# Optimization experiments

Hardware: AMD Instinct MI355X
Metric: run time of the kernel (lower is better)

Reference implementation:

```python
import jax, jax.numpy as jnp
import numpy as np

B, D, C, M = 16384, 512, 1000, 8


def setup_inputs() -> dict:
    key = jax.random.key(0)
    k1, k2, k3, k4 = jax.random.split(key, 4)
    x = jax.random.normal(k1, (B, D), dtype=jnp.float32)
    W = jax.random.normal(k2, (M, D, C), dtype=jnp.float32) * 0.02
    b = jax.random.normal(k3, (M, C), dtype=jnp.float32) * 0.02
    coefs = jax.random.uniform(k4, (M,), dtype=jnp.float32, minval=0.5, maxval=1.5)
    return {"x": x, "W": W, "b": b, "coefs": coefs}


def reference(x, W, b, coefs):
    # Per-model logits: [M, B, C]
    logits = jnp.einsum('bd,mdc->mbc', x, W) + b[:, None, :]
    pos = jnp.argmax(logits, axis=-1)  # [M, B] predicted class per model/sample
    rows = jnp.broadcast_to(jnp.arange(x.shape[0])[None, :], pos.shape)  # [M, B]
    # Weighted vote scatter-add: ans[j, pos[m, j]] += coefs[m]
    ans = jnp.zeros((x.shape[0], W.shape[2]), dtype=jnp.float32)
    ans = ans.at[rows, pos].add(jnp.broadcast_to(coefs[:, None], pos.shape))
    return ans / W.shape[0]
```

## Files before the change

### kernel.cpp

```cpp
#include <hip/hip_runtime.h>

#define B_N 16384
#define D_K 512
#define C_N 1000
#define CP 1024
#define M_N 8
#define GAP_EPS 1e-3f

typedef __attribute__((ext_vector_type(8))) _Float16 f16x8;
typedef __attribute__((ext_vector_type(4))) float f32x4;

typedef const __attribute__((address_space(1))) unsigned int* gptr_t;
typedef __attribute__((address_space(3))) unsigned int* lptr_t;

__device__ __forceinline__ void gload16(const void* g, void* l) {
    __builtin_amdgcn_global_load_lds((gptr_t)g, (lptr_t)l, 16, 0, 0);
}

#define BAR()        asm volatile("s_barrier" ::: "memory")
#define WAIT_LGKM0() asm volatile("s_waitcnt lgkmcnt(0)" ::: "memory")
#define WAIT_VM6()   asm volatile("s_waitcnt vmcnt(6)" ::: "memory")
#define WAIT_VM0()   asm volatile("s_waitcnt vmcnt(0)" ::: "memory")

__device__ __forceinline__ unsigned short h16(float f) {
    _Float16 h = (_Float16)f;
    return *(unsigned short*)&h;
}

__device__ __forceinline__ unsigned fkey32(float f) {
    unsigned u = __float_as_uint(f);
    return (u & 0x80000000u) ? ~u : (u | 0x80000000u);
}


__global__ __launch_bounds__(256) void ve_conv(const float* __restrict__ x,
        const float* __restrict__ W, unsigned short* __restrict__ xf,
        unsigned short* __restrict__ wt, unsigned int* __restrict__ cnts,
        float* __restrict__ out) {
    const int tid = threadIdx.x;
    if (blockIdx.x < 8192) {
        int i = blockIdx.x * 256 + tid;
        if (blockIdx.x == 0 && tid < M_N) cnts[tid] = 0u;
        float4 v = reinterpret_cast<const float4*>(x)[i];
        ushort4 h;
        h.x = h16(v.x); h.y = h16(v.y); h.z = h16(v.z); h.w = h16(v.w);
        reinterpret_cast<ushort4*>(xf)[i] = h;
    } else if (blockIdx.x < 9216) {
        __shared__ float t[64][65];
        const int b = blockIdx.x - 8192;
        const int c0 = (b & 15) * 64, k0 = ((b >> 4) & 7) * 64, m = b >> 7;
#pragma unroll
        for (int p = 0; p < 16; ++p) {
            int idx = p * 256 + tid;
            int kk = idx >> 6, cc = idx & 63;
            int c = c0 + cc;
            t[kk][cc] = (c < C_N) ? W[((size_t)m * D_K + k0 + kk) * C_N + c] : 0.f;
        }
        __syncthreads();
#pragma unroll
        for (int p = 0; p < 4; ++p) {
            int idx = p * 256 + tid;
            int cc = idx >> 4, kq = idx & 15;
            ushort4 h;
            h.x = h16(t[kq * 4 + 0][cc]); h.y = h16(t[kq * 4 + 1][cc]);
            h.z = h16(t[kq * 4 + 2][cc]); h.w = h16(t[kq * 4 + 3][cc]);
            size_t o = ((size_t)m * CP + c0 + cc) * D_K + k0 + kq * 4;
            *reinterpret_cast<ushort4*>(wt + o) = h;
        }
    } else {
        const int b = blockIdx.x - 9216;
        float4* po = reinterpret_cast<float4*>(out) + (size_t)b * 4000;
        const float4 z = make_float4(0.f, 0.f, 0.f, 0.f);
        for (int i = tid; i < 4000; i += 256) po[i] = z;
    }
}


__global__ __launch_bounds__(256, 2) void ve_gemm16d(
        const unsigned short* __restrict__ Xf, const unsigned short* __restrict__ WT,
        const float* __restrict__ bias, float4* __restrict__ part) {
    __shared__ unsigned short At[12288];
    __shared__ unsigned short Bt[24576];

    const int tid = threadIdx.x;
    const int l = tid & 63, w = tid >> 6;
    const int wr = w >> 1, wc = w & 1;
    const int l15 = l & 15, kg = l >> 4;
    const int bid = blockIdx.x;
    const int mb = bid & 7, ct = (bid >> 3) & 3, rt = bid >> 5;
    const int r0 = rt * 128, c0 = ct * 256;

    const int lhi = l >> 3, llo = l & 7;
    const int s3g = llo ^ lhi;
    const int srow16 = (lhi << 1) | (s3g >> 2);
    const int kgs = (s3g & 3) * 8;

    const unsigned short* xA0 = Xf + (size_t)(r0 +      w * 16 + srow16) * D_K + kgs;
    const unsigned short* xA1 = Xf + (size_t)(r0 + 64 + w * 16 + srow16) * D_K + kgs;
    const unsigned short* xB0 = WT + (size_t)(mb * CP + c0 +       w * 16 + srow16) * D_K + kgs;
    const unsigned short* xB1 = WT + (size_t)(mb * CP + c0 +  64 + w * 16 + srow16) * D_K + kgs;
    const unsigned short* xB2 = WT + (size_t)(mb * CP + c0 + 128 + w * 16 + srow16) * D_K + kgs;
    const unsigned short* xB3 = WT + (size_t)(mb * CP + c0 + 192 + w * 16 + srow16) * D_K + kgs;

    auto stage = [&](int t, int buf) {
        unsigned short* A = At + buf * 4096;
        unsigned short* B = Bt + buf * 8192;
        gload16(xA0 + t * 32, A + tid * 8);
        gload16(xA1 + t * 32, A + 2048 + tid * 8);
        gload16(xB0 + t * 32, B + tid * 8);
        gload16(xB1 + t * 32, B + 2048 + tid * 8);
        gload16(xB2 + t * 32, B + 4096 + tid * 8);
        gload16(xB3 + t * 32, B + 6144 + tid * 8);
    };

    auto ldsoff = [&](int row, int kc) {
        return (row >> 1) * 64 + (((((row & 1) << 2) | kc) ^ ((row >> 1) & 7)) * 8);
    };
    const char* aP[4]; const char* bP[8];
#pragma unroll
    for (int i = 0; i < 4; ++i)
        aP[i] = (const char*)At + 2 * ldsoff(wr * 64 + i * 16 + l15, kg);
#pragma unroll
    for (int j = 0; j < 8; ++j)
        bP[j] = (const char*)Bt + wc * 8192 + 2 * ldsoff(j * 16 + l15, kg);

    f32x4 acc[4][8];
#pragma unroll
    for (int i = 0; i < 4; ++i)
#pragma unroll
        for (int j = 0; j < 8; ++j) acc[i][j] = (f32x4){0.f, 0.f, 0.f, 0.f};

    stage(0, 0);
    stage(1, 1);
    WAIT_VM6();
    BAR();

#pragma unroll 1
    for (int t = 0; t < 16; ++t) {
        if (t < 14) stage(t + 2, (t + 2) % 3);
        const int curA = (t % 3) * 8192;
        const int curB = (t % 3) * 16384;

        f16x8 af[4], bf[8];
#pragma unroll
        for (int i = 0; i < 4; ++i) af[i] = *reinterpret_cast<const f16x8*>(aP[i] + curA);
#pragma unroll
        for (int j = 0; j < 8; ++j) bf[j] = *reinterpret_cast<const f16x8*>(bP[j] + curB);
        __builtin_amdgcn_s_setprio(1);
#pragma unroll
        for (int i = 0; i < 4; ++i)
#pragma unroll
            for (int j = 0; j < 8; ++j)
                acc[i][j] = __builtin_amdgcn_mfma_f32_16x16x32_f16(af[i], bf[j], acc[i][j], 0, 0, 0);
        __builtin_amdgcn_s_setprio(0);

        if (t < 14)       { WAIT_VM6(); }
        else if (t == 14) { WAIT_VM0(); }
        WAIT_LGKM0();
        BAR();
    }

    float4 (*wtop)[2] = reinterpret_cast<float4(*)[2]>(At);

    float bv[8]; int cg[8];
#pragma unroll
    for (int j = 0; j < 8; ++j) {
        int c = c0 + wc * 128 + j * 16 + l15;
        cg[j] = c;
        bv[j] = (c < C_N) ? bias[mb * C_N + c] : -1e30f;
    }
#pragma unroll
    for (int i = 0; i < 4; ++i) {
#pragma unroll
        for (int reg = 0; reg < 4; ++reg) {
            float v1 = acc[i][0][reg] + bv[0]; int i1 = cg[0];
            float v2 = -1e30f;
#pragma unroll
            for (int j = 1; j < 8; ++j) {
                float v = acc[i][j][reg] + bv[j];
                float mn = fminf(v, v1);
                v2 = fmaxf(v2, mn);
                i1 = (v > v1) ? cg[j] : i1;
                v1 = fmaxf(v1, v);
            }
#pragma unroll
            for (int mask = 1; mask < 16; mask <<= 1) {
                float ov1 = __shfl_xor(v1, mask);
                int   oi1 = __shfl_xor(i1, mask);
                float ov2 = __shfl_xor(v2, mask);
                float mn = fminf(v1, ov1);
                v2 = fmaxf(fmaxf(v2, ov2), mn);
                i1 = (ov1 > v1) ? oi1 : i1;
                v1 = fmaxf(v1, ov1);
            }
            if (l15 == 0) {
                int row = wr * 64 + i * 16 + (l >> 4) * 4 + reg;
                wtop[row][wc] = make_float4(v1, __int_as_float(i1), v2, 0.f);
            }
        }
    }
    __syncthreads();
    if (tid < 128) {
        float4 a = wtop[tid][0], b = wtop[tid][1];
        float v1, v2; int i1;
        if (b.x > a.x) {
            v1 = b.x; i1 = __float_as_int(b.y);
            v2 = fmaxf(a.x, b.z);
        } else {
            v1 = a.x; i1 = __float_as_int(a.y);
            v2 = fmaxf(b.x, a.z);
        }
        part[((size_t)mb * B_N + r0 + tid) * 4 + ct] =
            make_float4(v1, __int_as_float(i1), v2, 0.f);
    }
}


__global__ __launch_bounds__(128) void ve_flag4(const float4* __restrict__ part,
        unsigned int* __restrict__ wout, unsigned int* __restrict__ rlist,
        unsigned int* __restrict__ cnts, unsigned long long* __restrict__ fixkey) {
    int r = blockIdx.x * 128 + threadIdx.x;
#pragma unroll
    for (int m = 0; m < M_N; ++m) {
        float4 o = part[((size_t)m * B_N + r) * 4 + 0];
        float v1 = o.x; int i1 = __float_as_int(o.y); float v2 = o.z;
#pragma unroll
        for (int t = 1; t < 4; ++t) {
            float4 q = part[((size_t)m * B_N + r) * 4 + t];
            if (q.x > v1) {
                v2 = fmaxf(v1, fmaxf(q.z, v2));
                v1 = q.x; i1 = __float_as_int(q.y);
            } else {
                v2 = fmaxf(v2, q.x);
            }
        }
        if (v1 - v2 <= GAP_EPS) {
            wout[m * B_N + r] = (unsigned)i1 | 0x80000000u;
            fixkey[m * B_N + r] = 0ull;
            unsigned pos = atomicAdd(&cnts[m], 1u);
            rlist[m * B_N + pos] = (unsigned)r;
        } else {
            wout[m * B_N + r] = (unsigned)i1;
        }
    }
}


__global__ __launch_bounds__(256) void ve_exact_g(
        const float* __restrict__ x, const float* __restrict__ W,
        const float* __restrict__ bias, const unsigned int* __restrict__ rlist,
        const unsigned int* __restrict__ cnts, unsigned long long* __restrict__ fixkey) {
    __shared__ float xs[32][65];
    __shared__ float wsm[32][128];
    __shared__ int rg[64];
    const int ct = blockIdx.x, m = blockIdx.z;
    const int tid = threadIdx.x;
    const int tx = tid & 15, ty = tid >> 4;
    const int c0 = ct * 128;
    const unsigned nm = cnts[m];

    for (unsigned rb = blockIdx.y; rb * 64 < nm; rb += gridDim.y) {
        __syncthreads();
        if (tid < 64) {
            unsigned idx = rb * 64 + tid;
            rg[tid] = (idx < nm) ? (int)rlist[m * B_N + idx] : 0;
        }
        __syncthreads();

        float acc[4][8];
#pragma unroll
        for (int i = 0; i < 4; i++)
#pragma unroll
            for (int j = 0; j < 8; j++) acc[i][j] = 0.f;

        for (int kt = 0; kt < D_K; kt += 32) {
#pragma unroll
            for (int i = 0; i < 2; i++) {
                int li = tid + i * 256;
                int row = li >> 3, kq = li & 7;
                float4 v = *reinterpret_cast<const float4*>(
                        x + (size_t)rg[row] * D_K + kt + kq * 4);
                int kk = kq * 4;
                xs[kk + 0][row] = v.x; xs[kk + 1][row] = v.y;
                xs[kk + 2][row] = v.z; xs[kk + 3][row] = v.w;
            }
#pragma unroll
            for (int i = 0; i < 4; i++) {
                int li = tid + i * 256;
                int kk = li >> 5, cq = li & 31;
                int c = c0 + cq * 4;
                const float* p = W + ((size_t)(m * D_K + kt + kk)) * C_N + c;
                float4 v;
                if (c + 3 < C_N) v = *reinterpret_cast<const float4*>(p);
                else {
                    v.x = (c + 0 < C_N) ? p[0] : 0.f; v.y = (c + 1 < C_N) ? p[1] : 0.f;
                    v.z = (c + 2 < C_N) ? p[2] : 0.f; v.w = (c + 3 < C_N) ? p[3] : 0.f;
                }
                wsm[kk][cq * 4 + 0] = v.x; wsm[kk][cq * 4 + 1] = v.y;
                wsm[kk][cq * 4 + 2] = v.z; wsm[kk][cq * 4 + 3] = v.w;
            }
            __syncthreads();
            for (int kk = 0; kk < 32; kk++) {
                float a[4], bb[8];
#pragma unroll
                for (int i = 0; i < 4; i++) a[i] = xs[kk][ty + i * 16];
#pragma unroll
                for (int j = 0; j < 8; j++) bb[j] = wsm[kk][tx + j * 16];
#pragma unroll
                for (int i = 0; i < 4; i++)
#pragma unroll
                    for (int j = 0; j < 8; j++) acc[i][j] += a[i] * bb[j];
            }
            __syncthreads();
        }

        const float NEG_INF = -__builtin_huge_valf();
        float bv[8]; int cv[8];
#pragma unroll
        for (int j = 0; j < 8; j++) {
            int c = c0 + tx + j * 16;
            cv[j] = c;
            bv[j] = (c < C_N) ? bias[m * C_N + c] : 0.f;
        }
#pragma unroll
        for (int i = 0; i < 4; i++) {
            float best = NEG_INF; int bidx = 0x7fffffff;
#pragma unroll
            for (int j = 0; j < 8; j++) {
                int c = cv[j];
                float v = (c < C_N) ? (acc[i][j] + bv[j]) : NEG_INF;
                if (v > best || (v == best && c < bidx)) { best = v; bidx = c; }
            }
#pragma unroll
            for (int mask = 1; mask < 16; mask <<= 1) {
                float ov = __shfl_xor(best, mask);
                int oi = __shfl_xor(bidx, mask);
                if (ov > best || (ov == best && oi < bidx)) { best = ov; bidx = oi; }
            }
            unsigned slot = rb * 64 + ty + i * 16;
            if (tx == 0 && slot < nm) {
                unsigned long long key =
                    ((unsigned long long)fkey32(best) << 32) | (unsigned)(~(unsigned)bidx);
                atomicMax(fixkey + (size_t)m * B_N + rg[ty + i * 16], key);
            }
        }
    }
}

__global__ __launch_bounds__(128) void ve_votef(const unsigned int* __restrict__ wout,
        const unsigned long long* __restrict__ fixkey,
        const float* __restrict__ coefs, float* __restrict__ out) {
    int r = blockIdx.x * 128 + threadIdx.x;
#pragma unroll
    for (int m = 0; m < M_N; ++m) {
        unsigned wv = wout[m * B_N + r];
        int idx;
        if (wv & 0x80000000u) {
            unsigned long long k = fixkey[(size_t)m * B_N + r];
            idx = (int)(~(unsigned)k);
        } else {
            idx = (int)wv;
        }
        out[(size_t)r * C_N + idx] += coefs[m] * 0.125f;
    }
}


#define TM 128
#define TN 128
#define TK 32
#define CT 8

__global__ __launch_bounds__(256) void ve_zero_out(float* __restrict__ out, int n4) {
    int i = blockIdx.x * blockDim.x + threadIdx.x;
    const float4 z = make_float4(0.f, 0.f, 0.f, 0.f);
    for (; i < n4; i += gridDim.x * blockDim.x)
        reinterpret_cast<float4*>(out)[i] = z;
}

__global__ __launch_bounds__(256) void ve_gemm_argmax_fb(
        const float* __restrict__ x, const float* __restrict__ W,
        const float* __restrict__ bias, float2* __restrict__ part) {
    __shared__ float xs[TK][TM + 1];
    __shared__ float ws[TK][TN];
    const int ct = blockIdx.x, rt = blockIdx.y, m = blockIdx.z;
    const int tid = threadIdx.x;
    const int tx = tid & 15, ty = tid >> 4;
    const int r0 = rt * TM, c0 = ct * TN;
    float acc[8][8];
#pragma unroll
    for (int i = 0; i < 8; i++)
#pragma unroll
        for (int j = 0; j < 8; j++) acc[i][j] = 0.f;
    const float* xbase = x + (size_t)r0 * D_K;
    for (int kt = 0; kt < D_K; kt += TK) {
#pragma unroll
        for (int i = 0; i < 4; i++) {
            int li = tid + i * 256;
            int row = li >> 3, kq = li & 7;
            float4 v = *reinterpret_cast<const float4*>(xbase + (size_t)row * D_K + kt + kq * 4);
            int kk = kq * 4;
            xs[kk + 0][row] = v.x; xs[kk + 1][row] = v.y;
            xs[kk + 2][row] = v.z; xs[kk + 3][row] = v.w;
        }
#pragma unroll
        for (int i = 0; i < 4; i++) {
            int li = tid + i * 256;
            int kk = li >> 5, cq = li & 31;
            int c = c0 + cq * 4;
            const float* p = W + ((size_t)(m * D_K + kt + kk)) * C_N + c;
            float4 v;
            if (c + 3 < C_N) v = *reinterpret_cast<const float4*>(p);
            else {
                v.x = (c + 0 < C_N) ? p[0] : 0.f; v.y = (c + 1 < C_N) ? p[1] : 0.f;
                v.z = (c + 2 < C_N) ? p[2] : 0.f; v.w = (c + 3 < C_N) ? p[3] : 0.f;
            }
            ws[kk][cq * 4 + 0] = v.x; ws[kk][cq * 4 + 1] = v.y;
            ws[kk][cq * 4 + 2] = v.z; ws[kk][cq * 4 + 3] = v.w;
        }
        __syncthreads();
        for (int kk = 0; kk < TK; kk++) {
            float a[8], bb[8];
#pragma unroll
            for (int i = 0; i < 8; i++) a[i] = xs[kk][ty + i * 16];
#pragma unroll
            for (int j = 0; j < 8; j++) bb[j] = ws[kk][tx + j * 16];
#pragma unroll
            for (int i = 0; i < 8; i++)
#pragma unroll
                for (int j = 0; j < 8; j++) acc[i][j] += a[i] * bb[j];
        }
        __syncthreads();
    }
    const float NEG_INF = -__builtin_huge_valf();
    float bv[8]; int cv[8];
#pragma unroll
    for (int j = 0; j < 8; j++) {
        int c = c0 + tx + j * 16;
        cv[j] = c;
        bv[j] = (c < C_N) ? bias[m * C_N + c] : 0.f;
    }
#pragma unroll
    for (int i = 0; i < 8; i++) {
        int r = r0 + ty + i * 16;
        float best = NEG_INF; int bidx = 0x7fffffff;
#pragma unroll
        for (int j = 0; j < 8; j++) {
            int c = cv[j];
            float v = (c < C_N) ? (acc[i][j] + bv[j]) : NEG_INF;
            if (v > best || (v == best && c < bidx)) { best = v; bidx = c; }
        }
#pragma unroll
        for (int mask = 1; mask < 16; mask <<= 1) {
            float ov = __shfl_xor(best, mask);
            int oi = __shfl_xor(bidx, mask);
            if (ov > best || (ov == best && oi < bidx)) { best = ov; bidx = oi; }
        }
        if (tx == 0) part[((size_t)m * B_N + r) * CT + ct] = make_float2(best, __int_as_float(bidx));
    }
}

__global__ __launch_bounds__(256) void ve_vote_fb(const float2* __restrict__ part,
        const float* __restrict__ coefs, float* __restrict__ out) {
    int r = blockIdx.x * blockDim.x + threadIdx.x;
    if (r >= B_N) return;
    const float NEG_INF = -__builtin_huge_valf();
#pragma unroll
    for (int m = 0; m < M_N; m++) {
        float best = NEG_INF; int bidx = 0x7fffffff;
#pragma unroll
        for (int ctt = 0; ctt < CT; ctt++) {
            float2 p = part[((size_t)m * B_N + r) * CT + ctt];
            int oi = __float_as_int(p.y);
            if (p.x > best || (p.x == best && oi < bidx)) { best = p.x; bidx = oi; }
        }
        out[(size_t)r * C_N + bidx] += coefs[m] * 0.125f;
    }
}


extern "C" void kernel_launch(void* const* d_in, const int* in_sizes, int n_in,
                              void* d_out, int out_size, void* d_ws, size_t ws_size,
                              hipStream_t stream) {
    const float* x     = (const float*)d_in[0];
    const float* W     = (const float*)d_in[1];
    const float* bias  = (const float*)d_in[2];
    const float* coefs = (const float*)d_in[3];
    float* out = (float*)d_out;

    const size_t NEED = (57ull << 20) + 4096;
    if (ws_size >= NEED) {
        char* ws = (char*)d_ws;
        unsigned short*     Xf     = (unsigned short*)(ws);
        unsigned short*     WT16   = (unsigned short*)(ws + (16ull << 20));
        float4*             part   = (float4*)(ws + (24ull << 20));
        unsigned long long* fixkey = (unsigned long long*)(ws + (40ull << 20));
        unsigned int*       wout   = (unsigned int*)(ws + (48ull << 20));
        unsigned int*       rlist  = (unsigned int*)(ws + (48ull << 20) + (512ull << 10));
        unsigned int*       cnts   = (unsigned int*)(ws + (49ull << 20));

        ve_conv<<<10240, 256, 0, stream>>>(x, W, Xf, WT16, cnts, out);
        ve_gemm16d<<<4096, 256, 0, stream>>>(Xf, WT16, bias, part);
        ve_flag4<<<128, 128, 0, stream>>>(part, wout, rlist, cnts, fixkey);
        ve_exact_g<<<dim3(8, 8, 8), 256, 0, stream>>>(x, W, bias, rlist, cnts, fixkey);
        ve_votef<<<128, 128, 0, stream>>>(wout, fixkey, coefs, out);
    } else {
        float2* partf = (float2*)d_ws;
        ve_zero_out<<<2048, 256, 0, stream>>>(out, B_N * C_N / 4);
        dim3 grid(CT, B_N / TM, M_N);
        ve_gemm_argmax_fb<<<grid, 256, 0, stream>>>(x, W, bias, partf);
        ve_vote_fb<<<(B_N + 255) / 256, 256, 0, stream>>>(partf, coefs, out);
    }
}
```

Measured before the change: 311.2 us.

## Split GEMM tile across 8 waves with 64x64 per-wave subtiles

Doubles the GEMM workgroup from 256 to 512 threads in a 2x4 wave grid, so each wave owns a 64x64 output subtile instead of 64x128. This halves the accumulator registers per wave and the global-to-LDS loads per thread, aiming for more resident waves to hide latency. The per-row top-2 reduction now merges four wave partials instead of two, and the MFMA priority boosting is removed. In exchange each wave reads more LDS fragments per MFMA, and LDS usage per block may still cap how many blocks fit on a CU.

```diff
diff --git a/kernel.cpp b/kernel.cpp
--- a/kernel.cpp
+++ b/kernel.cpp
@@ -19,7 +19,7 @@
 
 #define BAR()        asm volatile("s_barrier" ::: "memory")
 #define WAIT_LGKM0() asm volatile("s_waitcnt lgkmcnt(0)" ::: "memory")
-#define WAIT_VM6()   asm volatile("s_waitcnt vmcnt(6)" ::: "memory")
+#define WAIT_VM3()   asm volatile("s_waitcnt vmcnt(3)" ::: "memory")
 #define WAIT_VM0()   asm volatile("s_waitcnt vmcnt(0)" ::: "memory")
 
 __device__ __forceinline__ unsigned short h16(float f) {
@@ -76,7 +76,7 @@
 }
 
 
-__global__ __launch_bounds__(256, 2) void ve_gemm16d(
+__global__ __launch_bounds__(512, 4) void ve_gemm16d(
         const unsigned short* __restrict__ Xf, const unsigned short* __restrict__ WT,
         const float* __restrict__ bias, float4* __restrict__ part) {
     __shared__ unsigned short At[12288];
@@ -84,7 +84,7 @@
 
     const int tid = threadIdx.x;
     const int l = tid & 63, w = tid >> 6;
-    const int wr = w >> 1, wc = w & 1;
+    const int wr = w >> 2, wc = w & 3;
     const int l15 = l & 15, kg = l >> 4;
     const int bid = blockIdx.x;
     const int mb = bid & 7, ct = (bid >> 3) & 3, rt = bid >> 5;
@@ -92,47 +92,40 @@
 
     const int lhi = l >> 3, llo = l & 7;
     const int s3g = llo ^ lhi;
-    const int srow16 = (lhi << 1) | (s3g >> 2);
+    const int w16s = w * 16 + ((lhi << 1) | (s3g >> 2));
     const int kgs = (s3g & 3) * 8;
 
-    const unsigned short* xA0 = Xf + (size_t)(r0 +      w * 16 + srow16) * D_K + kgs;
-    const unsigned short* xA1 = Xf + (size_t)(r0 + 64 + w * 16 + srow16) * D_K + kgs;
-    const unsigned short* xB0 = WT + (size_t)(mb * CP + c0 +       w * 16 + srow16) * D_K + kgs;
-    const unsigned short* xB1 = WT + (size_t)(mb * CP + c0 +  64 + w * 16 + srow16) * D_K + kgs;
-    const unsigned short* xB2 = WT + (size_t)(mb * CP + c0 + 128 + w * 16 + srow16) * D_K + kgs;
-    const unsigned short* xB3 = WT + (size_t)(mb * CP + c0 + 192 + w * 16 + srow16) * D_K + kgs;
+    const unsigned short* xA   = Xf + (size_t)(r0 + w16s) * D_K + kgs;
+    const unsigned short* xBs0 = WT + (size_t)(mb * CP + c0 +       w16s) * D_K + kgs;
+    const unsigned short* xBs1 = WT + (size_t)(mb * CP + c0 + 128 + w16s) * D_K + kgs;
 
     auto stage = [&](int t, int buf) {
-        unsigned short* A = At + buf * 4096;
-        unsigned short* B = Bt + buf * 8192;
-        gload16(xA0 + t * 32, A + tid * 8);
-        gload16(xA1 + t * 32, A + 2048 + tid * 8);
-        gload16(xB0 + t * 32, B + tid * 8);
-        gload16(xB1 + t * 32, B + 2048 + tid * 8);
-        gload16(xB2 + t * 32, B + 4096 + tid * 8);
-        gload16(xB3 + t * 32, B + 6144 + tid * 8);
+        gload16(xA   + t * 32, At + buf * 4096 + tid * 8);
+        gload16(xBs0 + t * 32, Bt + buf * 8192 + tid * 8);
+        gload16(xBs1 + t * 32, Bt + buf * 8192 + 4096 + tid * 8);
     };
 
     auto ldsoff = [&](int row, int kc) {
         return (row >> 1) * 64 + (((((row & 1) << 2) | kc) ^ ((row >> 1) & 7)) * 8);
     };
-    const char* aP[4]; const char* bP[8];
+    const char* aP[4]; const char* bP[4];
 #pragma unroll
     for (int i = 0; i < 4; ++i)
         aP[i] = (const char*)At + 2 * ldsoff(wr * 64 + i * 16 + l15, kg);
 #pragma unroll
-    for (int j = 0; j < 8; ++j)
-        bP[j] = (const char*)Bt + wc * 8192 + 2 * ldsoff(j * 16 + l15, kg);
-
-    f32x4 acc[4][8];
+    for (int j = 0; j < 4; ++j)
+        bP[j] = (const char*)Bt + (wc >> 1) * 8192
+              + 2 * ldsoff((wc & 1) * 64 + j * 16 + l15, kg);
+
+    f32x4 acc[4][4];
 #pragma unroll
     for (int i = 0; i < 4; ++i)
 #pragma unroll
-        for (int j = 0; j < 8; ++j) acc[i][j] = (f32x4){0.f, 0.f, 0.f, 0.f};
+        for (int j = 0; j < 4; ++j) acc[i][j] = (f32x4){0.f, 0.f, 0.f, 0.f};
 
     stage(0, 0);
     stage(1, 1);
-    WAIT_VM6();
+    WAIT_VM3();
     BAR();
 
 #pragma unroll 1
@@ -141,31 +134,29 @@
         const int curA = (t % 3) * 8192;
         const int curB = (t % 3) * 16384;
 
-        f16x8 af[4], bf[8];
+        f16x8 af[4], bf[4];
 #pragma unroll
         for (int i = 0; i < 4; ++i) af[i] = *reinterpret_cast<const f16x8*>(aP[i] + curA);
 #pragma unroll
-        for (int j = 0; j < 8; ++j) bf[j] = *reinterpret_cast<const f16x8*>(bP[j] + curB);
-        __builtin_amdgcn_s_setprio(1);
+        for (int j = 0; j < 4; ++j) bf[j] = *reinterpret_cast<const f16x8*>(bP[j] + curB);
 #pragma unroll
         for (int i = 0; i < 4; ++i)
 #pragma unroll
-            for (int j = 0; j < 8; ++j)
+            for (int j = 0; j < 4; ++j)
                 acc[i][j] = __builtin_amdgcn_mfma_f32_16x16x32_f16(af[i], bf[j], acc[i][j], 0, 0, 0);
-        __builtin_amdgcn_s_setprio(0);
-
-        if (t < 14)       { WAIT_VM6(); }
+
+        if (t < 14)       { WAIT_VM3(); }
         else if (t == 14) { WAIT_VM0(); }
         WAIT_LGKM0();
         BAR();
     }
 
-    float4 (*wtop)[2] = reinterpret_cast<float4(*)[2]>(At);
-
-    float bv[8]; int cg[8];
-#pragma unroll
-    for (int j = 0; j < 8; ++j) {
-        int c = c0 + wc * 128 + j * 16 + l15;
+    float4 (*wtop)[4] = reinterpret_cast<float4(*)[4]>(At);
+
+    float bv[4]; int cg[4];
+#pragma unroll
+    for (int j = 0; j < 4; ++j) {
+        int c = c0 + wc * 64 + j * 16 + l15;
         cg[j] = c;
         bv[j] = (c < C_N) ? bias[mb * C_N + c] : -1e30f;
     }
@@ -176,7 +167,7 @@
             float v1 = acc[i][0][reg] + bv[0]; int i1 = cg[0];
             float v2 = -1e30f;
 #pragma unroll
-            for (int j = 1; j < 8; ++j) {
+            for (int j = 1; j < 4; ++j) {
                 float v = acc[i][j][reg] + bv[j];
                 float mn = fminf(v, v1);
                 v2 = fmaxf(v2, mn);
@@ -201,14 +192,17 @@
     }
     __syncthreads();
     if (tid < 128) {
-        float4 a = wtop[tid][0], b = wtop[tid][1];
-        float v1, v2; int i1;
-        if (b.x > a.x) {
-            v1 = b.x; i1 = __float_as_int(b.y);
-            v2 = fmaxf(a.x, b.z);
-        } else {
-            v1 = a.x; i1 = __float_as_int(a.y);
-            v2 = fmaxf(b.x, a.z);
+        float4 o = wtop[tid][0];
+        float v1 = o.x; int i1 = __float_as_int(o.y); float v2 = o.z;
+#pragma unroll
+        for (int s = 1; s < 4; ++s) {
+            float4 q = wtop[tid][s];
+            if (q.x > v1) {
+                v2 = fmaxf(v1, fmaxf(q.z, v2));
+                v1 = q.x; i1 = __float_as_int(q.y);
+            } else {
+                v2 = fmaxf(v2, q.x);
+            }
         }
         part[((size_t)mb * B_N + r0 + tid) * 4 + ct] =
             make_float4(v1, __int_as_float(i1), v2, 0.f);
@@ -500,7 +494,7 @@
         unsigned int*       cnts   = (unsigned int*)(ws + (49ull << 20));
 
         ve_conv<<<10240, 256, 0, stream>>>(x, W, Xf, WT16, cnts, out);
-        ve_gemm16d<<<4096, 256, 0, stream>>>(Xf, WT16, bias, part);
+        ve_gemm16d<<<4096, 512, 0, stream>>>(Xf, WT16, bias, part);
         ve_flag4<<<128, 128, 0, stream>>>(part, wout, rlist, cnts, fixkey);
         ve_exact_g<<<dim3(8, 8, 8), 256, 0, stream>>>(x, W, bias, rlist, cnts, fixkey);
         ve_votef<<<128, 128, 0, stream>>>(wout, fixkey, coefs, out);
```

Result: slower. 323.6 us (+4.0%).
